# Kernel tuning notes

Measured on AMD Instinct MI355X. Metric: run time of the kernel, lower is better.

## Reference

```python
import jax, jax.numpy as jnp
import numpy as np

N_ATOMS = 500000
N_BONDS = 1000000
NODE = 128
EDGE = 16
OUT = 128
DEGREES = (1, 2, 3, 4)
COUNTS = (50000, 150000, 200000, 100000)  # sums to N_ATOMS
EPS = 1e-5


def setup_inputs() -> dict:
    key = jax.random.key(0)
    ks = jax.random.split(key, 16)
    atom_repr = jax.random.normal(ks[0], (N_ATOMS, NODE), dtype=jnp.float32)
    bond_repr = jax.random.normal(ks[1], (N_BONDS, EDGE), dtype=jnp.float32)
    # first column of each degree group's atom index list is the node's own id;
    # the union of first columns is a permutation of 0..N_ATOMS-1 (every node in exactly one group)
    perm = jax.random.permutation(ks[2], N_ATOMS)
    inp = {"atom_repr": atom_repr, "bond_repr": bond_repr}
    off = 0
    for i, (d, n) in enumerate(zip(DEGREES, COUNTS)):
        own = perm[off:off + n][:, None]
        nbrs = jax.random.randint(ks[3 + 2 * i], (n, d), 0, N_ATOMS)
        inp[f"atom_idx_{d}"] = jnp.concatenate([own, nbrs], axis=1).astype(jnp.int32)
        inp[f"bond_idx_{d}"] = jax.random.randint(ks[4 + 2 * i], (n, d), 0, N_BONDS).astype(jnp.int32)
        off += n
    # parameters (torch Linear weights stored here as [in, out])
    s = 1.0 / np.sqrt(NODE)
    inp["W_self"] = jax.random.uniform(ks[11], (NODE, OUT), jnp.float32, -s, s)
    sd = 1.0 / np.sqrt(NODE + EDGE)
    inp["W1"] = jax.random.uniform(ks[12], (NODE + EDGE, OUT), jnp.float32, -sd, sd)
    inp["W2"] = jax.random.uniform(ks[13], (NODE + EDGE, OUT), jnp.float32, -sd, sd)
    inp["W3"] = jax.random.uniform(ks[14], (NODE + EDGE, OUT), jnp.float32, -sd, sd)
    inp["W4"] = jax.random.uniform(ks[15], (NODE + EDGE, OUT), jnp.float32, -sd, sd)
    inp["bias"] = jnp.zeros((1, OUT), dtype=jnp.float32)
    return inp


def reference(atom_repr, bond_repr, W_self, W1, W2, W3, W4, bias,
              atom_idx_1, atom_idx_2, atom_idx_3, atom_idx_4,
              bond_idx_1, bond_idx_2, bond_idx_3, bond_idx_4):
    Ws = (W1, W2, W3, W4)
    aidxs = (atom_idx_1, atom_idx_2, atom_idx_3, atom_idx_4)
    bidxs = (bond_idx_1, bond_idx_2, bond_idx_3, bond_idx_4)
    n = atom_repr.shape[0]
    neighbor_repr = jnp.zeros((n, OUT), dtype=atom_repr.dtype)
    for W, aidx, bidx in zip(Ws, aidxs, bidxs):
        a_sum = atom_repr[aidx].sum(axis=1)      # [n_d, NODE] (includes self, per original)
        b_sum = bond_repr[bidx].sum(axis=1)      # [n_d, EDGE]
        act = jnp.concatenate([a_sum, b_sum], axis=1) @ W  # [n_d, OUT]
        # scatter back to node order (equivalent to concat + argsort by atoms[0])
        neighbor_repr = neighbor_repr.at[aidx[:, 0]].set(act)
    self_repr = atom_repr @ W_self
    x = self_repr + neighbor_repr + bias
    # BatchNorm1d(affine=False), training mode: biased batch stats
    mean = x.mean(axis=0)
    var = x.var(axis=0)
    x = (x - mean) * jax.lax.rsqrt(var + EPS)
    return jax.nn.relu(x)
```

## Files before the change

### kernel.cpp

```cpp
#include <hip/hip_runtime.h>
#include <hip/hip_bf16.h>
#include <math.h>

#define N_ATOMS 500000
#define EPS 1e-5f
#define LDA 296

#define NB1 55
#define NB2 249
#define NB3 443
#define NB4 277
#define NBLK 1024

#define SEG_ELEMS 36864

typedef __attribute__((ext_vector_type(8))) short short8;
typedef __attribute__((ext_vector_type(8))) unsigned short ushort8v;
typedef __attribute__((ext_vector_type(4))) float floatx4;

__device__ __forceinline__ unsigned short f2bf(float f) {
    unsigned int x = __float_as_uint(f);
    x += 0x7FFF + ((x >> 16) & 1);
    return (unsigned short)(x >> 16);
}

__device__ __forceinline__ float bf2f(unsigned short u) {
    return __uint_as_float(((unsigned int)u) << 16);
}

__device__ __forceinline__ float4 add4(float4 a, float4 b) {
    return make_float4(a.x + b.x, a.y + b.y, a.z + b.z, a.w + b.w);
}

__device__ __forceinline__ void st_bf4(unsigned short* p, float4 v) {
    ushort4 u;
    u.x = f2bf(v.x); u.y = f2bf(v.y); u.z = f2bf(v.z); u.w = f2bf(v.w);
    *reinterpret_cast<ushort4*>(p) = u;
}

__global__ __launch_bounds__(256) void gdc_cvt(const float* __restrict__ a,
                                               unsigned short* __restrict__ o)
{
    const size_t nchunks = (size_t)N_ATOMS * 128 / 8;
    size_t idx = (size_t)blockIdx.x * 256 + threadIdx.x;
    const size_t stride = (size_t)gridDim.x * 256;
    for (; idx < nchunks; idx += stride) {
        floatx4 x0 = __builtin_nontemporal_load(((const floatx4*)a) + idx * 2);
        floatx4 x1 = __builtin_nontemporal_load(((const floatx4*)a) + idx * 2 + 1);
        ushort8v v;
        v[0] = f2bf(x0[0]); v[1] = f2bf(x0[1]); v[2] = f2bf(x0[2]); v[3] = f2bf(x0[3]);
        v[4] = f2bf(x1[0]); v[5] = f2bf(x1[1]); v[6] = f2bf(x1[2]); v[7] = f2bf(x1[3]);
        *(((ushort8v*)o) + idx) = v;
    }
}

__global__ __launch_bounds__(256) void gdc_pack(
    const float* __restrict__ W1, const float* __restrict__ W2,
    const float* __restrict__ W3, const float* __restrict__ W4,
    const float* __restrict__ Wself, unsigned short* __restrict__ packed)
{
    const int t = blockIdx.x * 256 + threadIdx.x;
    if (t >= 4 * 9 * 8 * 64) return;
    const int d    = t / 4608;
    const int r    = t % 4608;
    const int ks   = r / 512;
    const int nt   = (r % 512) / 64;
    const int lane = r % 64;
    const float* Wd = (d == 0) ? W1 : (d == 1) ? W2 : (d == 2) ? W3 : W4;
    const int col = nt * 16 + (lane & 15);
    short8 v;
    #pragma unroll
    for (int j = 0; j < 8; ++j) {
        const int k = ks * 32 + ((lane >> 4) << 3) + j;
        float w = 0.f;
        if (k < 144)      w = Wd[k * 128 + col];
        else if (k < 272) w = Wself[(k - 144) * 128 + col];
        v[j] = (short)f2bf(w);
    }
    *reinterpret_cast<short8*>(packed + (size_t)d * SEG_ELEMS
                               + ((size_t)(ks * 8 + nt) * 64 + lane) * 8) = v;
}

template <int DEG, bool BF, bool XBF>
__device__ __forceinline__ void block_loop(
    const float* __restrict__ atom, const unsigned short* __restrict__ abf,
    const float* __restrict__ bond,
    const int* __restrict__ aidx, const int* __restrict__ bidx,
    const unsigned short* __restrict__ pw,
    float* __restrict__ out, unsigned short* __restrict__ xout,
    unsigned short* __restrict__ A, int* __restrict__ own_lds,
    int n, int lb, int nb, int tid, int lane, int wv)
{
    const int m    = tid >> 4;
    const int q16  = tid & 15;
    const int ccol = lane & 15;
    const int crow = lane >> 4;
    const int nbase = wv * 16;

    short8 bfr[9];
    #pragma unroll
    for (int ks = 0; ks < 9; ++ks)
        bfr[ks] = ((const short8*)pw)[(ks * 8 + wv) * 64 + lane];

    float psum = 0.f, psq = 0.f;
    const int tiles = (n + 31) >> 5;
    const int nmax  = n - 1;

    ushort8v rawb[DEG + 1];
    float4 rawf[DEG + 1][2];
    float2 rb[DEG];
    int own_r;
    int ni[DEG + 1];

    {
        const int i = min((lb << 5) + m, nmax);
        const int* ar = aidx + (size_t)i * (DEG + 1);
        #pragma unroll
        for (int j = 0; j <= DEG; ++j) ni[j] = ar[j];
        own_r = ni[0];
        #pragma unroll
        for (int j = 0; j <= DEG; ++j) {
            if (BF) {
                rawb[j] = *reinterpret_cast<const ushort8v*>(abf + (size_t)ni[j] * 128 + q16 * 8);
            } else {
                const float4* pp = (const float4*)(atom + (size_t)ni[j] * 128 + q16 * 8);
                rawf[j][0] = pp[0]; rawf[j][1] = pp[1];
            }
        }
        if (q16 < 8) {
            const int* br = bidx + (size_t)i * DEG;
            #pragma unroll
            for (int j = 0; j < DEG; ++j)
                rb[j] = *(const float2*)(bond + (size_t)br[j] * 16 + q16 * 2);
        }
        const int t1 = min(lb + nb, tiles - 1);
        const int i1 = min((t1 << 5) + m, nmax);
        const int* ar1 = aidx + (size_t)i1 * (DEG + 1);
        #pragma unroll
        for (int j = 0; j <= DEG; ++j) ni[j] = ar1[j];
    }

    int k = 0;
    for (int t = lb; t < tiles; t += nb, ++k) {
        unsigned short* Ab = A + (k & 1) * (32 * LDA);
        int* ob = own_lds + (k & 1) * 32;

        {
            unsigned short* rowp = Ab + m * LDA;
            if (BF) {
                *reinterpret_cast<ushort8v*>(rowp + 144 + q16 * 8) = rawb[0];
                float s[8];
                #pragma unroll
                for (int e = 0; e < 8; ++e) s[e] = bf2f(rawb[0][e]);
                #pragma unroll
                for (int j = 1; j <= DEG; ++j)
                    #pragma unroll
                    for (int e = 0; e < 8; ++e) s[e] += bf2f(rawb[j][e]);
                ushort8v sm;
                #pragma unroll
                for (int e = 0; e < 8; ++e) sm[e] = f2bf(s[e]);
                *reinterpret_cast<ushort8v*>(rowp + q16 * 8) = sm;
            } else {
                st_bf4(rowp + 144 + q16 * 8 + 0, rawf[0][0]);
                st_bf4(rowp + 144 + q16 * 8 + 4, rawf[0][1]);
                float4 s0 = rawf[0][0], s1 = rawf[0][1];
                #pragma unroll
                for (int j = 1; j <= DEG; ++j) {
                    s0 = add4(s0, rawf[j][0]); s1 = add4(s1, rawf[j][1]);
                }
                st_bf4(rowp + q16 * 8 + 0, s0);
                st_bf4(rowp + q16 * 8 + 4, s1);
            }
            if (q16 < 8) {
                float bx = rb[0].x, by = rb[0].y;
                #pragma unroll
                for (int j = 1; j < DEG; ++j) { bx += rb[j].x; by += rb[j].y; }
                rowp[128 + q16 * 2]     = f2bf(bx);
                rowp[128 + q16 * 2 + 1] = f2bf(by);
            }
            if (q16 == 0) ob[m] = own_r;
        }
        __syncthreads();

        if (t + nb < tiles) {
            const int i = min(((t + nb) << 5) + m, nmax);
            own_r = ni[0];
            #pragma unroll
            for (int j = 0; j <= DEG; ++j) {
                if (BF) {
                    rawb[j] = *reinterpret_cast<const ushort8v*>(abf + (size_t)ni[j] * 128 + q16 * 8);
                } else {
                    const float4* pp = (const float4*)(atom + (size_t)ni[j] * 128 + q16 * 8);
                    rawf[j][0] = pp[0]; rawf[j][1] = pp[1];
                }
            }
            if (q16 < 8) {
                const int* br = bidx + (size_t)i * DEG;
                #pragma unroll
                for (int j = 0; j < DEG; ++j)
                    rb[j] = *(const float2*)(bond + (size_t)br[j] * 16 + q16 * 2);
            }
            const int t2 = min(t + 2 * nb, tiles - 1);
            const int i2 = min((t2 << 5) + m, nmax);
            const int* ar2 = aidx + (size_t)i2 * (DEG + 1);
            #pragma unroll
            for (int j = 0; j <= DEG; ++j) ni[j] = ar2[j];
        }

        floatx4 acc0 = (floatx4){0.f, 0.f, 0.f, 0.f};
        floatx4 acc1 = (floatx4){0.f, 0.f, 0.f, 0.f};
        #pragma unroll
        for (int ks = 0; ks < 9; ++ks) {
            const short8 af0 = *(const short8*)&Ab[ccol * LDA + ks * 32 + (crow << 3)];
            const short8 af1 = *(const short8*)&Ab[(16 + ccol) * LDA + ks * 32 + (crow << 3)];
            acc0 = __builtin_amdgcn_mfma_f32_16x16x32_bf16(af0, bfr[ks], acc0, 0, 0, 0);
            acc1 = __builtin_amdgcn_mfma_f32_16x16x32_bf16(af1, bfr[ks], acc1, 0, 0, 0);
        }

        const int i0 = t << 5;
        const int4 o0 = *reinterpret_cast<const int4*>(&ob[crow * 4]);
        const int4 o1 = *reinterpret_cast<const int4*>(&ob[16 + crow * 4]);
        const int owns0[4] = {o0.x, o0.y, o0.z, o0.w};
        const int owns1[4] = {o1.x, o1.y, o1.z, o1.w};
        #pragma unroll
        for (int rr = 0; rr < 4; ++rr) {
            const int row = crow * 4 + rr;
            if (i0 + row < n) {
                const float v = acc0[rr];
                if (XBF) {
                    const unsigned short u = f2bf(v);
                    const float vr = bf2f(u);
                    xout[(size_t)owns0[rr] * 128 + nbase + ccol] = u;
                    psum += vr; psq += vr * vr;
                } else {
                    out[(size_t)owns0[rr] * 128 + nbase + ccol] = v;
                    psum += v; psq += v * v;
                }
            }
            if (i0 + 16 + row < n) {
                const float v = acc1[rr];
                if (XBF) {
                    const unsigned short u = f2bf(v);
                    const float vr = bf2f(u);
                    xout[(size_t)owns1[rr] * 128 + nbase + ccol] = u;
                    psum += vr; psq += vr * vr;
                } else {
                    out[(size_t)owns1[rr] * 128 + nbase + ccol] = v;
                    psum += v; psq += v * v;
                }
            }
        }
    }

    __syncthreads();

    float* redS = reinterpret_cast<float*>(A);
    float* redQ = redS + 128;
    {
        float s = psum, q = psq;
        s += __shfl_xor(s, 16, 64); s += __shfl_xor(s, 32, 64);
        q += __shfl_xor(q, 16, 64); q += __shfl_xor(q, 32, 64);
        if (lane < 16) {
            redS[nbase + lane] = s;
            redQ[nbase + lane] = q;
        }
    }
}

template <bool BF, bool XBF>
__global__ __launch_bounds__(512, 4) void gdc_mfma(
    const float* __restrict__ atom, const unsigned short* __restrict__ abf,
    const float* __restrict__ bond,
    const int* __restrict__ a1, const int* __restrict__ b1,
    const int* __restrict__ a2, const int* __restrict__ b2,
    const int* __restrict__ a3, const int* __restrict__ b3,
    const int* __restrict__ a4, const int* __restrict__ b4,
    const unsigned short* __restrict__ packedW,
    float* __restrict__ out, unsigned short* __restrict__ xout,
    float* __restrict__ sumPart, float* __restrict__ sqPart)
{
    __shared__ __align__(16) unsigned short A[2 * 32 * LDA];
    __shared__ __align__(16) int own_lds[2 * 32];

    const int tid  = threadIdx.x;
    const int wv   = tid >> 6;
    const int lane = tid & 63;
    const int blk  = blockIdx.x;

    int n, lb, nb, deg;
    const int* aidx; const int* bidx;
    if (blk < NB1)                 { deg = 1; n =  50000; lb = blk;                 nb = NB1; aidx = a1; bidx = b1; }
    else if (blk < NB1+NB2)        { deg = 2; n = 150000; lb = blk-NB1;             nb = NB2; aidx = a2; bidx = b2; }
    else if (blk < NB1+NB2+NB3)    { deg = 3; n = 200000; lb = blk-(NB1+NB2);       nb = NB3; aidx = a3; bidx = b3; }
    else                           { deg = 4; n = 100000; lb = blk-(NB1+NB2+NB3);   nb = NB4; aidx = a4; bidx = b4; }

    const unsigned short* pw = packedW + (size_t)(deg - 1) * SEG_ELEMS;

    {
        const int mm = tid >> 4, qq = tid & 15;
        if (qq >= 8) {
            ushort2 z; z.x = 0; z.y = 0;
            *reinterpret_cast<ushort2*>(&A[mm * LDA + 272 + (qq - 8) * 2]) = z;
            *reinterpret_cast<ushort2*>(&A[32 * LDA + mm * LDA + 272 + (qq - 8) * 2]) = z;
        }
    }
    __syncthreads();

    switch (deg) {
    case 1:  block_loop<1, BF, XBF>(atom, abf, bond, aidx, bidx, pw, out, xout, A, own_lds, n, lb, nb, tid, lane, wv); break;
    case 2:  block_loop<2, BF, XBF>(atom, abf, bond, aidx, bidx, pw, out, xout, A, own_lds, n, lb, nb, tid, lane, wv); break;
    case 3:  block_loop<3, BF, XBF>(atom, abf, bond, aidx, bidx, pw, out, xout, A, own_lds, n, lb, nb, tid, lane, wv); break;
    default: block_loop<4, BF, XBF>(atom, abf, bond, aidx, bidx, pw, out, xout, A, own_lds, n, lb, nb, tid, lane, wv); break;
    }

    __syncthreads();
    const float* redS = reinterpret_cast<const float*>(A);
    if (tid < 128)      sumPart[(size_t)blk * 128 + tid] = redS[tid];
    else if (tid < 256) sqPart[(size_t)blk * 128 + (tid - 128)] = redS[tid];
}

__global__ void gdc_stats(const float* __restrict__ sumPart,
                          const float* __restrict__ sqPart,
                          float* __restrict__ mv)
{
    const int c = blockIdx.x;
    const int j = threadIdx.x;
    __shared__ float rs[256], rq[256];
    float s = 0.f, q = 0.f;
    for (int b = j; b < NBLK; b += 256) {
        s += sumPart[(size_t)b * 128 + c];
        q += sqPart[(size_t)b * 128 + c];
    }
    rs[j] = s; rq[j] = q;
    __syncthreads();
    for (int off = 128; off > 0; off >>= 1) {
        if (j < off) { rs[j] += rs[j + off]; rq[j] += rq[j + off]; }
        __syncthreads();
    }
    if (j == 0) {
        const float mean = rs[0] / (float)N_ATOMS;
        const float var  = rq[0] / (float)N_ATOMS - mean * mean;
        mv[c]       = mean;
        mv[128 + c] = rsqrtf(var + EPS);
    }
}

__global__ __launch_bounds__(256) void gdc_norm_bf(const unsigned short* __restrict__ x,
                                                   float* __restrict__ out,
                                                   const float* __restrict__ mv)
{
    const size_t total8 = (size_t)N_ATOMS * 128 / 8;
    size_t idx = (size_t)blockIdx.x * 256 + threadIdx.x;
    const int c = (int)((idx * 8) & 127);
    const float4 m0 = *(const float4*)(mv + c);
    const float4 m1 = *(const float4*)(mv + c + 4);
    const float4 i0 = *(const float4*)(mv + 128 + c);
    const float4 i1 = *(const float4*)(mv + 128 + c + 4);
    const size_t stride = (size_t)gridDim.x * 256;
    for (; idx < total8; idx += stride) {
        const ushort8v v = *(((const ushort8v*)x) + idx);
        floatx4 o0, o1;
        o0[0] = fmaxf(0.f, (bf2f(v[0]) - m0.x) * i0.x);
        o0[1] = fmaxf(0.f, (bf2f(v[1]) - m0.y) * i0.y);
        o0[2] = fmaxf(0.f, (bf2f(v[2]) - m0.z) * i0.z);
        o0[3] = fmaxf(0.f, (bf2f(v[3]) - m0.w) * i0.w);
        o1[0] = fmaxf(0.f, (bf2f(v[4]) - m1.x) * i1.x);
        o1[1] = fmaxf(0.f, (bf2f(v[5]) - m1.y) * i1.y);
        o1[2] = fmaxf(0.f, (bf2f(v[6]) - m1.z) * i1.z);
        o1[3] = fmaxf(0.f, (bf2f(v[7]) - m1.w) * i1.w);
        __builtin_nontemporal_store(o0, ((floatx4*)out) + idx * 2);
        __builtin_nontemporal_store(o1, ((floatx4*)out) + idx * 2 + 1);
    }
}

__global__ __launch_bounds__(256) void gdc_norm(float* __restrict__ out,
                                                const float* __restrict__ mv)
{
    const size_t total4 = (size_t)N_ATOMS * 128 / 4;
    size_t idx = (size_t)blockIdx.x * 256 + threadIdx.x;
    const int c = (int)((idx * 4) & 127);
    const float4 m  = *(const float4*)(mv + c);
    const float4 iv = *(const float4*)(mv + 128 + c);
    const size_t stride = (size_t)gridDim.x * 256;
    for (; idx < total4; idx += stride) {
        floatx4 v = __builtin_nontemporal_load(((const floatx4*)out) + idx);
        v[0] = fmaxf(0.f, (v[0] - m.x) * iv.x);
        v[1] = fmaxf(0.f, (v[1] - m.y) * iv.y);
        v[2] = fmaxf(0.f, (v[2] - m.z) * iv.z);
        v[3] = fmaxf(0.f, (v[3] - m.w) * iv.w);
        __builtin_nontemporal_store(v, ((floatx4*)out) + idx);
    }
}

extern "C" void kernel_launch(void* const* d_in, const int* in_sizes, int n_in,
                              void* d_out, int out_size, void* d_ws, size_t ws_size,
                              hipStream_t stream) {
    const float* atom  = (const float*)d_in[0];
    const float* bond  = (const float*)d_in[1];
    const int*   a1    = (const int*)d_in[2];
    const int*   b1    = (const int*)d_in[3];
    const int*   a2    = (const int*)d_in[4];
    const int*   b2    = (const int*)d_in[5];
    const int*   a3    = (const int*)d_in[6];
    const int*   b3    = (const int*)d_in[7];
    const int*   a4    = (const int*)d_in[8];
    const int*   b4    = (const int*)d_in[9];
    const float* Wself = (const float*)d_in[10];
    const float* W1    = (const float*)d_in[11];
    const float* W2    = (const float*)d_in[12];
    const float* W3    = (const float*)d_in[13];
    const float* W4    = (const float*)d_in[14];
    float* out = (float*)d_out;

    const size_t abf_bytes  = (size_t)N_ATOMS * 128 * sizeof(unsigned short);
    const size_t xbf_bytes  = abf_bytes;
    const size_t pack_bytes = 4 * SEG_ELEMS * sizeof(unsigned short);
    const size_t part_bytes = (size_t)NBLK * 128 * sizeof(float);
    const size_t need_full  = abf_bytes + xbf_bytes + pack_bytes + 2 * part_bytes + 1024;
    const size_t need_bf    = abf_bytes + pack_bytes + 2 * part_bytes + 1024;

    if (ws_size >= need_full) {
        char* p = (char*)d_ws;
        unsigned short* abf     = (unsigned short*)p;  p += abf_bytes;
        unsigned short* xbf     = (unsigned short*)p;  p += xbf_bytes;
        unsigned short* packedW = (unsigned short*)p;  p += pack_bytes;
        float* sumPart = (float*)p;                    p += part_bytes;
        float* sqPart  = (float*)p;                    p += part_bytes;
        float* mv      = (float*)p;

        hipLaunchKernelGGL(gdc_cvt, dim3(2048), dim3(256), 0, stream, atom, abf);
        hipLaunchKernelGGL(gdc_pack, dim3((4*9*8*64 + 255)/256), dim3(256), 0, stream,
                           W1, W2, W3, W4, Wself, packedW);
        hipLaunchKernelGGL((gdc_mfma<true, true>), dim3(NBLK), dim3(512), 0, stream,
                           atom, abf, bond, a1, b1, a2, b2, a3, b3, a4, b4,
                           packedW, out, xbf, sumPart, sqPart);
        hipLaunchKernelGGL(gdc_stats, dim3(128), dim3(256), 0, stream,
                           sumPart, sqPart, mv);
        hipLaunchKernelGGL(gdc_norm_bf, dim3(2048), dim3(256), 0, stream, xbf, out, mv);
    } else if (ws_size >= need_bf) {
        char* p = (char*)d_ws;
        unsigned short* abf     = (unsigned short*)p;  p += abf_bytes;
        unsigned short* packedW = (unsigned short*)p;  p += pack_bytes;
        float* sumPart = (float*)p;                    p += part_bytes;
        float* sqPart  = (float*)p;                    p += part_bytes;
        float* mv      = (float*)p;

        hipLaunchKernelGGL(gdc_cvt, dim3(2048), dim3(256), 0, stream, atom, abf);
        hipLaunchKernelGGL(gdc_pack, dim3((4*9*8*64 + 255)/256), dim3(256), 0, stream,
                           W1, W2, W3, W4, Wself, packedW);
        hipLaunchKernelGGL((gdc_mfma<true, false>), dim3(NBLK), dim3(512), 0, stream,
                           atom, abf, bond, a1, b1, a2, b2, a3, b3, a4, b4,
                           packedW, out, (unsigned short*)nullptr, sumPart, sqPart);
        hipLaunchKernelGGL(gdc_stats, dim3(128), dim3(256), 0, stream,
                           sumPart, sqPart, mv);
        hipLaunchKernelGGL(gdc_norm, dim3(2048), dim3(256), 0, stream, out, mv);
    } else {
        char* p = (char*)d_ws;
        unsigned short* packedW = (unsigned short*)p;  p += pack_bytes;
        float* sumPart = (float*)p;                    p += part_bytes;
        float* sqPart  = (float*)p;                    p += part_bytes;
        float* mv      = (float*)p;

        hipLaunchKernelGGL(gdc_pack, dim3((4*9*8*64 + 255)/256), dim3(256), 0, stream,
                           W1, W2, W3, W4, Wself, packedW);
        hipLaunchKernelGGL((gdc_mfma<false, false>), dim3(NBLK), dim3(512), 0, stream,
                           atom, (const unsigned short*)nullptr, bond,
                           a1, b1, a2, b2, a3, b3, a4, b4,
                           packedW, out, (unsigned short*)nullptr, sumPart, sqPart);
        hipLaunchKernelGGL(gdc_stats, dim3(128), dim3(256), 0, stream,
                           sumPart, sqPart, mv);
        hipLaunchKernelGGL(gdc_norm, dim3(2048), dim3(256), 0, stream, out, mv);
    }
}
```

Before: 304.3 us.

## Double row tile to 64 rows per block iteration with four MFMA M-tiles

Each block iteration now processes 64 destination rows instead of 32. Every thread gathers two rows, and each wave issues four 16x16x32 MFMAs per K step against the same register-resident weight fragment. The goal is more memory-level parallelism in flight per thread, fewer loop iterations and barriers, and all 16 lanes per row used for bond gathers. In exchange, LDS use per block doubles (about 76KB for the A buffers), which can cut the number of resident blocks, and register pressure grows, which risks occupancy under launch_bounds(512,4).

```diff
diff --git a/kernel.cpp b/kernel.cpp
--- a/kernel.cpp
+++ b/kernel.cpp
@@ -93,6 +93,7 @@
 {
     const int m    = tid >> 4;
     const int q16  = tid & 15;
+    const int qb   = (q16 & 7) * 2;
     const int ccol = lane & 15;
     const int crow = lane >> 4;
     const int nbase = wv * 16;
@@ -103,150 +104,165 @@
         bfr[ks] = ((const short8*)pw)[(ks * 8 + wv) * 64 + lane];
 
     float psum = 0.f, psq = 0.f;
-    const int tiles = (n + 31) >> 5;
+    const int tiles = (n + 63) >> 6;
     const int nmax  = n - 1;
 
-    ushort8v rawb[DEG + 1];
-    float4 rawf[DEG + 1][2];
+    ushort8v rawa[DEG + 1], rawc[DEG + 1];
+    float4 rafa[DEG + 1][2], rafc[DEG + 1][2];
     float2 rb[DEG];
-    int own_r;
-    int ni[DEG + 1];
+    int nia[DEG + 1], nib[DEG + 1];
+    int owna_r, ownb_r;
 
     {
-        const int i = min((lb << 5) + m, nmax);
-        const int* ar = aidx + (size_t)i * (DEG + 1);
-        #pragma unroll
-        for (int j = 0; j <= DEG; ++j) ni[j] = ar[j];
-        own_r = ni[0];
+        const int ia = min((lb << 6) + m, nmax);
+        const int ib = min((lb << 6) + 32 + m, nmax);
+        const int* ar = aidx + (size_t)ia * (DEG + 1);
+        const int* br = aidx + (size_t)ib * (DEG + 1);
+        #pragma unroll
+        for (int j = 0; j <= DEG; ++j) { nia[j] = ar[j]; nib[j] = br[j]; }
+        owna_r = nia[0]; ownb_r = nib[0];
         #pragma unroll
         for (int j = 0; j <= DEG; ++j) {
             if (BF) {
-                rawb[j] = *reinterpret_cast<const ushort8v*>(abf + (size_t)ni[j] * 128 + q16 * 8);
+                rawa[j] = *reinterpret_cast<const ushort8v*>(abf + (size_t)nia[j] * 128 + q16 * 8);
+                rawc[j] = *reinterpret_cast<const ushort8v*>(abf + (size_t)nib[j] * 128 + q16 * 8);
             } else {
-                const float4* pp = (const float4*)(atom + (size_t)ni[j] * 128 + q16 * 8);
-                rawf[j][0] = pp[0]; rawf[j][1] = pp[1];
-            }
-        }
-        if (q16 < 8) {
-            const int* br = bidx + (size_t)i * DEG;
+                const float4* pa = (const float4*)(atom + (size_t)nia[j] * 128 + q16 * 8);
+                const float4* pc = (const float4*)(atom + (size_t)nib[j] * 128 + q16 * 8);
+                rafa[j][0] = pa[0]; rafa[j][1] = pa[1];
+                rafc[j][0] = pc[0]; rafc[j][1] = pc[1];
+            }
+        }
+        {
+            const int ibd = (q16 < 8) ? ia : ib;
+            const int* bp = bidx + (size_t)ibd * DEG;
             #pragma unroll
             for (int j = 0; j < DEG; ++j)
-                rb[j] = *(const float2*)(bond + (size_t)br[j] * 16 + q16 * 2);
+                rb[j] = *(const float2*)(bond + (size_t)bp[j] * 16 + qb);
         }
         const int t1 = min(lb + nb, tiles - 1);
-        const int i1 = min((t1 << 5) + m, nmax);
-        const int* ar1 = aidx + (size_t)i1 * (DEG + 1);
-        #pragma unroll
-        for (int j = 0; j <= DEG; ++j) ni[j] = ar1[j];
+        const int ia1 = min((t1 << 6) + m, nmax);
+        const int ib1 = min((t1 << 6) + 32 + m, nmax);
+        const int* ar1 = aidx + (size_t)ia1 * (DEG + 1);
+        const int* br1 = aidx + (size_t)ib1 * (DEG + 1);
+        #pragma unroll
+        for (int j = 0; j <= DEG; ++j) { nia[j] = ar1[j]; nib[j] = br1[j]; }
     }
 
     int k = 0;
     for (int t = lb; t < tiles; t += nb, ++k) {
-        unsigned short* Ab = A + (k & 1) * (32 * LDA);
-        int* ob = own_lds + (k & 1) * 32;
+        unsigned short* Ab = A + (k & 1) * (64 * LDA);
+        int* ob = own_lds + (k & 1) * 64;
 
         {
-            unsigned short* rowp = Ab + m * LDA;
+            unsigned short* rowa = Ab + m * LDA;
+            unsigned short* rowc = Ab + (m + 32) * LDA;
             if (BF) {
-                *reinterpret_cast<ushort8v*>(rowp + 144 + q16 * 8) = rawb[0];
-                float s[8];
-                #pragma unroll
-                for (int e = 0; e < 8; ++e) s[e] = bf2f(rawb[0][e]);
+                *reinterpret_cast<ushort8v*>(rowa + 144 + q16 * 8) = rawa[0];
+                *reinterpret_cast<ushort8v*>(rowc + 144 + q16 * 8) = rawc[0];
+                float sa[8], sc[8];
+                #pragma unroll
+                for (int e = 0; e < 8; ++e) { sa[e] = bf2f(rawa[0][e]); sc[e] = bf2f(rawc[0][e]); }
                 #pragma unroll
                 for (int j = 1; j <= DEG; ++j)
                     #pragma unroll
-                    for (int e = 0; e < 8; ++e) s[e] += bf2f(rawb[j][e]);
-                ushort8v sm;
-                #pragma unroll
-                for (int e = 0; e < 8; ++e) sm[e] = f2bf(s[e]);
-                *reinterpret_cast<ushort8v*>(rowp + q16 * 8) = sm;
+                    for (int e = 0; e < 8; ++e) { sa[e] += bf2f(rawa[j][e]); sc[e] += bf2f(rawc[j][e]); }
+                ushort8v va, vc;
+                #pragma unroll
+                for (int e = 0; e < 8; ++e) { va[e] = f2bf(sa[e]); vc[e] = f2bf(sc[e]); }
+                *reinterpret_cast<ushort8v*>(rowa + q16 * 8) = va;
+                *reinterpret_cast<ushort8v*>(rowc + q16 * 8) = vc;
             } else {
-                st_bf4(rowp + 144 + q16 * 8 + 0, rawf[0][0]);
-                st_bf4(rowp + 144 + q16 * 8 + 4, rawf[0][1]);
-                float4 s0 = rawf[0][0], s1 = rawf[0][1];
+                st_bf4(rowa + 144 + q16 * 8 + 0, rafa[0][0]);
+                st_bf4(rowa + 144 + q16 * 8 + 4, rafa[0][1]);
+                st_bf4(rowc + 144 + q16 * 8 + 0, rafc[0][0]);
+                st_bf4(rowc + 144 + q16 * 8 + 4, rafc[0][1]);
+                float4 a0 = rafa[0][0], a1 = rafa[0][1], c0 = rafc[0][0], c1 = rafc[0][1];
                 #pragma unroll
                 for (int j = 1; j <= DEG; ++j) {
-                    s0 = add4(s0, rawf[j][0]); s1 = add4(s1, rawf[j][1]);
+                    a0 = add4(a0, rafa[j][0]); a1 = add4(a1, rafa[j][1]);
+                    c0 = add4(c0, rafc[j][0]); c1 = add4(c1, rafc[j][1]);
                 }
-                st_bf4(rowp + q16 * 8 + 0, s0);
-                st_bf4(rowp + q16 * 8 + 4, s1);
-            }
-            if (q16 < 8) {
+                st_bf4(rowa + q16 * 8 + 0, a0);
+                st_bf4(rowa + q16 * 8 + 4, a1);
+                st_bf4(rowc + q16 * 8 + 0, c0);
+                st_bf4(rowc + q16 * 8 + 4, c1);
+            }
+            {
+                unsigned short* rowbd = (q16 < 8) ? rowa : rowc;
                 float bx = rb[0].x, by = rb[0].y;
                 #pragma unroll
                 for (int j = 1; j < DEG; ++j) { bx += rb[j].x; by += rb[j].y; }
-                rowp[128 + q16 * 2]     = f2bf(bx);
-                rowp[128 + q16 * 2 + 1] = f2bf(by);
-            }
-            if (q16 == 0) ob[m] = own_r;
+                rowbd[128 + qb]     = f2bf(bx);
+                rowbd[128 + qb + 1] = f2bf(by);
+            }
+            if (q16 == 0) { ob[m] = owna_r; ob[m + 32] = ownb_r; }
         }
         __syncthreads();
 
         if (t + nb < tiles) {
-            const int i = min(((t + nb) << 5) + m, nmax);
-            own_r = ni[0];
+            const int ia = min(((t + nb) << 6) + m, nmax);
+            const int ib = min(((t + nb) << 6) + 32 + m, nmax);
+            owna_r = nia[0]; ownb_r = nib[0];
             #pragma unroll
             for (int j = 0; j <= DEG; ++j) {
                 if (BF) {
-                    rawb[j] = *reinterpret_cast<const ushort8v*>(abf + (size_t)ni[j] * 128 + q16 * 8);
+                    rawa[j] = *reinterpret_cast<const ushort8v*>(abf + (size_t)nia[j] * 128 + q16 * 8);
+                    rawc[j] = *reinterpret_cast<const ushort8v*>(abf + (size_t)nib[j] * 128 + q16 * 8);
                 } else {
-                    const float4* pp = (const float4*)(atom + (size_t)ni[j] * 128 + q16 * 8);
-                    rawf[j][0] = pp[0]; rawf[j][1] = pp[1];
+                    const float4* pa = (const float4*)(atom + (size_t)nia[j] * 128 + q16 * 8);
+                    const float4* pc = (const float4*)(atom + (size_t)nib[j] * 128 + q16 * 8);
+                    rafa[j][0] = pa[0]; rafa[j][1] = pa[1];
+                    rafc[j][0] = pc[0]; rafc[j][1] = pc[1];
                 }
             }
-            if (q16 < 8) {
-                const int* br = bidx + (size_t)i * DEG;
+            {
+                const int ibd = (q16 < 8) ? ia : ib;
+                const int* bp = bidx + (size_t)ibd * DEG;
                 #pragma unroll
                 for (int j = 0; j < DEG; ++j)
-                    rb[j] = *(const float2*)(bond + (size_t)br[j] * 16 + q16 * 2);
+                    rb[j] = *(const float2*)(bond + (size_t)bp[j] * 16 + qb);
             }
             const int t2 = min(t + 2 * nb, tiles - 1);
-            const int i2 = min((t2 << 5) + m, nmax);
-            const int* ar2 = aidx + (size_t)i2 * (DEG + 1);
+            const int ia2 = min((t2 << 6) + m, nmax);
+            const int ib2 = min((t2 << 6) + 32 + m, nmax);
+            const int* ar2 = aidx + (size_t)ia2 * (DEG + 1);
+            const int* br2 = aidx + (size_t)ib2 * (DEG + 1);
             #pragma unroll
-            for (int j = 0; j <= DEG; ++j) ni[j] = ar2[j];
-        }
-
-        floatx4 acc0 = (floatx4){0.f, 0.f, 0.f, 0.f};
-        floatx4 acc1 = (floatx4){0.f, 0.f, 0.f, 0.f};
+            for (int j = 0; j <= DEG; ++j) { nia[j] = ar2[j]; nib[j] = br2[j]; }
+        }
+
+        floatx4 acc[4];
+        #pragma unroll
+        for (int mt = 0; mt < 4; ++mt) acc[mt] = (floatx4){0.f, 0.f, 0.f, 0.f};
         #pragma unroll
         for (int ks = 0; ks < 9; ++ks) {
-            const short8 af0 = *(const short8*)&Ab[ccol * LDA + ks * 32 + (crow << 3)];
-            const short8 af1 = *(const short8*)&Ab[(16 + ccol) * LDA + ks * 32 + (crow << 3)];
-            acc0 = __builtin_amdgcn_mfma_f32_16x16x32_bf16(af0, bfr[ks], acc0, 0, 0, 0);
-            acc1 = __builtin_amdgcn_mfma_f32_16x16x32_bf16(af1, bfr[ks], acc1, 0, 0, 0);
-        }
-
-        const int i0 = t << 5;
-        const int4 o0 = *reinterpret_cast<const int4*>(&ob[crow * 4]);
-        const int4 o1 = *reinterpret_cast<const int4*>(&ob[16 + crow * 4]);
-        const int owns0[4] = {o0.x, o0.y, o0.z, o0.w};
-        const int owns1[4] = {o1.x, o1.y, o1.z, o1.w};
-        #pragma unroll
-        for (int rr = 0; rr < 4; ++rr) {
-            const int row = crow * 4 + rr;
-            if (i0 + row < n) {
-                const float v = acc0[rr];
-                if (XBF) {
-                    const unsigned short u = f2bf(v);
-                    const float vr = bf2f(u);
-                    xout[(size_t)owns0[rr] * 128 + nbase + ccol] = u;
-                    psum += vr; psq += vr * vr;
-                } else {
-                    out[(size_t)owns0[rr] * 128 + nbase + ccol] = v;
-                    psum += v; psq += v * v;
-                }
-            }
-            if (i0 + 16 + row < n) {
-                const float v = acc1[rr];
-                if (XBF) {
-                    const unsigned short u = f2bf(v);
-                    const float vr = bf2f(u);
-                    xout[(size_t)owns1[rr] * 128 + nbase + ccol] = u;
-                    psum += vr; psq += vr * vr;
-                } else {
-                    out[(size_t)owns1[rr] * 128 + nbase + ccol] = v;
-                    psum += v; psq += v * v;
+            #pragma unroll
+            for (int mt = 0; mt < 4; ++mt) {
+                const short8 af = *(const short8*)&Ab[(mt * 16 + ccol) * LDA + ks * 32 + (crow << 3)];
+                acc[mt] = __builtin_amdgcn_mfma_f32_16x16x32_bf16(af, bfr[ks], acc[mt], 0, 0, 0);
+            }
+        }
+
+        const int i0 = t << 6;
+        #pragma unroll
+        for (int mt = 0; mt < 4; ++mt) {
+            const int4 o4 = *reinterpret_cast<const int4*>(&ob[mt * 16 + crow * 4]);
+            const int owns[4] = {o4.x, o4.y, o4.z, o4.w};
+            #pragma unroll
+            for (int rr = 0; rr < 4; ++rr) {
+                const int row = mt * 16 + crow * 4 + rr;
+                if (i0 + row < n) {
+                    const float v = acc[mt][rr];
+                    if (XBF) {
+                        const unsigned short u = f2bf(v);
+                        const float vr = bf2f(u);
+                        xout[(size_t)owns[rr] * 128 + nbase + ccol] = u;
+                        psum += vr; psq += vr * vr;
+                    } else {
+                        out[(size_t)owns[rr] * 128 + nbase + ccol] = v;
+                        psum += v; psq += v * v;
+                    }
                 }
             }
         }
@@ -279,8 +295,8 @@
     float* __restrict__ out, unsigned short* __restrict__ xout,
     float* __restrict__ sumPart, float* __restrict__ sqPart)
 {
-    __shared__ __align__(16) unsigned short A[2 * 32 * LDA];
-    __shared__ __align__(16) int own_lds[2 * 32];
+    __shared__ __align__(16) unsigned short A[2 * 64 * LDA];
+    __shared__ __align__(16) int own_lds[2 * 64];
 
     const int tid  = threadIdx.x;
     const int wv   = tid >> 6;
@@ -297,12 +313,10 @@
     const unsigned short* pw = packedW + (size_t)(deg - 1) * SEG_ELEMS;
 
     {
-        const int mm = tid >> 4, qq = tid & 15;
-        if (qq >= 8) {
-            ushort2 z; z.x = 0; z.y = 0;
-            *reinterpret_cast<ushort2*>(&A[mm * LDA + 272 + (qq - 8) * 2]) = z;
-            *reinterpret_cast<ushort2*>(&A[32 * LDA + mm * LDA + 272 + (qq - 8) * 2]) = z;
-        }
+        const int mm = tid >> 3, qq = tid & 7;
+        ushort2 z; z.x = 0; z.y = 0;
+        *reinterpret_cast<ushort2*>(&A[mm * LDA + 272 + qq * 2]) = z;
+        *reinterpret_cast<ushort2*>(&A[64 * LDA + mm * LDA + 272 + qq * 2]) = z;
     }
     __syncthreads();
 
```

Measured after the change: 325.9 us. 1.07x slower.
